# Kernel optimization log

Hardware: AMD Instinct MI355X
Metric: run time of the kernel (lower is better)

## Reference

```python
import jax, jax.numpy as jnp
import numpy as np

B, S, D, H = 2, 2048, 1024, 16


def setup_inputs() -> dict:
    key = jax.random.key(0)
    kq, kk, kv, kw = jax.random.split(key, 4)
    Q = jax.random.normal(kq, (B, S, D), dtype=jnp.float32)
    K = jax.random.normal(kk, (B, S, D), dtype=jnp.float32)
    V = jax.random.normal(kv, (B, S, D), dtype=jnp.float32)
    Wo = jax.random.normal(kw, (D, D), dtype=jnp.float32) * (1.0 / np.sqrt(D))
    return {"Q": Q, "K": K, "V": V, "Wo": Wo, "num_heads": H}


def reference(Q, K, V, Wo, num_heads):
    b, s, d = Q.shape
    dk = d // num_heads
    # split heads: [B,S,D] -> [B,H,S,dk]
    q = Q.reshape(b, s, num_heads, dk).transpose(0, 2, 1, 3)
    k = K.reshape(b, s, num_heads, dk).transpose(0, 2, 1, 3)
    v = V.reshape(b, s, num_heads, dk).transpose(0, 2, 1, 3)
    scale = 1.0 / jnp.sqrt(jnp.asarray(dk, dtype=q.dtype))
    logits = jnp.einsum('bhqd,bhkd->bhqk', q, k) * scale  # [B,H,S,S]
    probs = jax.nn.softmax(logits, axis=-1).astype(q.dtype)
    o = jnp.einsum('bhqk,bhkd->bhqd', probs, v)  # [B,H,S,dk]
    o = o.transpose(0, 2, 1, 3).reshape(b, s, d)  # concat heads
    # O = einsum('d dkh, ... dkh -> ... d', Wo, scores) == scores @ Wo^T
    return jnp.einsum('dk,bsk->bsd', Wo, o)
```

## Files before the change

kernel.cpp:

```cpp
#include <hip/hip_runtime.h>
#include <hip/hip_bf16.h>

#define B_ 2
#define S_ 2048
#define D_ 1024
#define H_ 16
#define DK_ 64

typedef __hip_bfloat16 bf16;
typedef short v8s __attribute__((ext_vector_type(8)));
typedef short v4s __attribute__((ext_vector_type(4)));
typedef float v4f __attribute__((ext_vector_type(4)));
typedef float v16f __attribute__((ext_vector_type(16)));
typedef int   v4i __attribute__((ext_vector_type(4)));
typedef int   v2i __attribute__((ext_vector_type(2)));

static __device__ __forceinline__ v16f mfma32(v8s a, v8s b, v16f c) {
  return __builtin_amdgcn_mfma_f32_32x32x16_bf16(a, b, c, 0, 0, 0);
}
static __device__ __forceinline__ void gl2lds16(const void* g, void* l) {
  __builtin_amdgcn_global_load_lds((const __attribute__((address_space(1))) void*)g,
                                   (__attribute__((address_space(3))) void*)l,
                                   16, 0, 0);
}
static __device__ __forceinline__ short f2bf(float x) {
  return (short)__builtin_bit_cast(unsigned short, __float2bfloat16(x));
}
static __device__ __forceinline__ int pk2f(float lo, float hi) {
  unsigned a = __builtin_bit_cast(unsigned, lo) + 0x8000u;
  unsigned b = __builtin_bit_cast(unsigned, hi) + 0x8000u;
  return (int)__builtin_amdgcn_perm(b, a, 0x07060302u);
}
static __device__ __forceinline__ float bf2f(short s) {
  return __builtin_bit_cast(float, ((unsigned)(unsigned short)s) << 16);
}

__global__ __launch_bounds__(256) void pre_kernel(
    const float* __restrict__ K, const float* __restrict__ V,
    const float* __restrict__ Wo, bf16* __restrict__ Kb,
    bf16* __restrict__ Vt, bf16* __restrict__ Wb)
{
  __shared__ __align__(16) bf16 td[64 * 72];
  const int t = threadIdx.x;
  const int bx = blockIdx.x;

  if (bx < 2048) {
    const int idx = bx * 256 + t;
    const int seg = idx & 7;
    const int rest = idx >> 3;
    const int h = rest & 15;
    const int bs = rest >> 4;
    const float* src = K + (size_t)bs * D_ + h * 64 + seg * 8;
    v4f x = *(const v4f*)src, y = *(const v4f*)(src + 4);
    v8s r;
    r[0]=f2bf(x[0]); r[1]=f2bf(x[1]); r[2]=f2bf(x[2]); r[3]=f2bf(x[3]);
    r[4]=f2bf(y[0]); r[5]=f2bf(y[1]); r[6]=f2bf(y[2]); r[7]=f2bf(y[3]);
    const int b = bs >> 11, s = bs & 2047;
    *(v8s*)(Kb + ((size_t)(b * H_ + h) * S_ + s) * DK_ + seg * 8) = r;
  } else if (bx < 3072) {
    const int idx = bx - 2048;
    const int bh = idx >> 5, b = bh >> 4, h = bh & 15;
    const int s0 = (idx & 31) * 64;
    const int srow = t >> 2;
    const int cs = t & 3;
    const float* vp = V + (size_t)(b * S_ + s0 + srow) * D_ + h * 64 + cs * 16;
#pragma unroll
    for (int j = 0; j < 4; j++) {
      v4f x = *(const v4f*)(vp + j * 4);
#pragma unroll
      for (int jj = 0; jj < 4; jj++)
        td[(cs * 16 + j * 4 + jj) * 72 + srow] = __float2bfloat16(x[jj]);
    }
    __syncthreads();
    const int d = t >> 2;
#pragma unroll
    for (int a2 = 0; a2 < 4; a2++) {
      const int pos = cs * 16 + a2 * 4;
      const int g = pos >> 5;
      const int a = (pos >> 2) & 7;
      const int kbase = g * 32 + ((a >> 2) << 4) + ((a & 1) << 3) + (((a >> 1) & 1) << 2);
      v4s val = *(const v4s*)(td + d * 72 + kbase);
      *(v4s*)(Vt + ((size_t)bh * DK_ + d) * S_ + s0 + pos) = val;
    }
  } else {
    const int i = ((bx - 3072) * 256 + t) * 4;
    v4f a = *(const v4f*)(Wo + i);
    v4s r;
    r[0]=f2bf(a[0]); r[1]=f2bf(a[1]); r[2]=f2bf(a[2]); r[3]=f2bf(a[3]);
    *(v4s*)((short*)Wb + i) = r;
  }
}

__global__ __launch_bounds__(256, 4) void attn4_kernel(
    const float* __restrict__ Q, const bf16* __restrict__ Kb,
    const bf16* __restrict__ Vt, bf16* __restrict__ Op0,
    bf16* __restrict__ Op1, float* __restrict__ Lp)
{
  __shared__ __align__(16) bf16 kk[2][64 * 64];
  __shared__ __align__(16) bf16 vv[2][64 * 64];

  const int t = threadIdx.x;
  const int w = t >> 6, l = t & 63, h2 = l >> 5, ln = l & 31;

  const int bid = blockIdx.x;
  const int xcd = bid & 7;
  const int idx = bid >> 3;
  const int bh  = xcd * 4 + (idx >> 5);
  const int rest = idx & 31;
  const int qt = rest & 15, z = rest >> 4;

  const int b = bh >> 4, h = bh & 15;
  const int qbase = qt * 128 + w * 32;
  const int kb0 = z << 10;

  const bf16* Kbh = Kb + (size_t)bh * (S_ * DK_);
  const bf16* Vbh = Vt + (size_t)bh * (DK_ * S_);

  const float sc = 0.18033688011112042f;
  v8s bq[4];
  {
    const float* qp = Q + ((size_t)b * S_ + qbase + ln) * D_ + h * DK_ + h2 * 8;
#pragma unroll
    for (int c = 0; c < 4; c++) {
      v4f x = *(const v4f*)(qp + c * 16);
      v4f y = *(const v4f*)(qp + c * 16 + 4);
      v4i r = { pk2f(x[0]*sc, x[1]*sc), pk2f(x[2]*sc, x[3]*sc),
                pk2f(y[0]*sc, y[1]*sc), pk2f(y[2]*sc, y[3]*sc) };
      bq[c] = __builtin_bit_cast(v8s, r);
    }
  }

  v16f Z;
#pragma unroll
  for (int r = 0; r < 16; r++) Z[r] = 0.f;

  v16f accA, accB;
#pragma unroll
  for (int r = 0; r < 16; r++) { accA[r] = 0.f; accB[r] = 0.f; }
  float lpart = 0.f;

#pragma unroll
  for (int j = 0; j < 2; j++) {
    const int flat = j * 256 + t, row = flat >> 3, sp = flat & 7;
    gl2lds16(Kbh + (size_t)(kb0 + row) * DK_ + ((sp ^ (row & 7)) * 8), &kk[0][flat * 8]);
    gl2lds16(Vbh + (size_t)row * S_ + kb0 + ((sp ^ (row & 7)) * 8), &vv[0][flat * 8]);
  }

  int it = 0;
  for (int kb = kb0; kb < kb0 + 1024; kb += 64, it ^= 1) {
    __syncthreads();
    if (kb + 64 < kb0 + 1024) {
#pragma unroll
      for (int j = 0; j < 2; j++) {
        const int flat = j * 256 + t, row = flat >> 3, sp = flat & 7;
        gl2lds16(Kbh + (size_t)(kb + 64 + row) * DK_ + ((sp ^ (row & 7)) * 8),
                 &kk[it ^ 1][flat * 8]);
        gl2lds16(Vbh + (size_t)row * S_ + (kb + 64) + ((sp ^ (row & 7)) * 8),
                 &vv[it ^ 1][flat * 8]);
      }
    }
    const bf16* kc_ = kk[it];
    const bf16* vc_ = vv[it];

    v16f s0, s1;
    __builtin_amdgcn_s_setprio(1);
#pragma unroll
    for (int c = 0; c < 4; c++) {
      const int sd = 2 * c + h2;
      v8s a0 = *(const v8s*)(kc_ + ln * 64 + ((sd ^ (ln & 7)) * 8));
      v8s a1 = *(const v8s*)(kc_ + (32 + ln) * 64 + ((sd ^ (ln & 7)) * 8));
      if (c == 0) {
        s0 = mfma32(a0, bq[0], Z);
        s1 = mfma32(a1, bq[0], Z);
      } else {
        s0 = mfma32(a0, bq[c], s0);
        s1 = mfma32(a1, bq[c], s1);
      }
    }
    __builtin_amdgcn_s_setprio(0);

    float p0[16], p1[16];
#pragma unroll
    for (int r = 0; r < 16; r++) { p0[r] = exp2f(s0[r]); p1[r] = exp2f(s1[r]); }
    float suA = 0.f, suB = 0.f;
#pragma unroll
    for (int r = 0; r < 16; r++) { suA += p0[r]; suB += p1[r]; }
    lpart += suA + suB;

    v4i i00 = { pk2f(p0[0],p0[1]),  pk2f(p0[2],p0[3]),  pk2f(p0[4],p0[5]),  pk2f(p0[6],p0[7]) };
    v4i i01 = { pk2f(p0[8],p0[9]),  pk2f(p0[10],p0[11]),pk2f(p0[12],p0[13]),pk2f(p0[14],p0[15]) };
    v4i i10 = { pk2f(p1[0],p1[1]),  pk2f(p1[2],p1[3]),  pk2f(p1[4],p1[5]),  pk2f(p1[6],p1[7]) };
    v4i i11 = { pk2f(p1[8],p1[9]),  pk2f(p1[10],p1[11]),pk2f(p1[12],p1[13]),pk2f(p1[14],p1[15]) };
    v8s pb00 = __builtin_bit_cast(v8s, i00);
    v8s pb01 = __builtin_bit_cast(v8s, i01);
    v8s pb10 = __builtin_bit_cast(v8s, i10);
    v8s pb11 = __builtin_bit_cast(v8s, i11);

    __builtin_amdgcn_s_setprio(1);
#pragma unroll
    for (int st = 0; st < 2; st++) {
#pragma unroll
      for (int kc = 0; kc < 2; kc++) {
        const int q = st * 4 + kc * 2 + h2;
        v8s avA = *(const v8s*)(vc_ + ln * 64 + ((q ^ (ln & 7)) * 8));
        v8s avB = *(const v8s*)(vc_ + (32 + ln) * 64 + ((q ^ (ln & 7)) * 8));
        v8s pb = st ? (kc ? pb11 : pb10) : (kc ? pb01 : pb00);
        accA = mfma32(avA, pb, accA);
        accB = mfma32(avB, pb, accB);
      }
    }
    __builtin_amdgcn_s_setprio(0);
  }

  __syncthreads();
  const float lfull = lpart + __shfl_xor(lpart, 32);
  bf16* epw = &kk[0][0] + w * 2048;
#pragma unroll
  for (int r = 0; r < 16; r += 4) {
    const int off = 4 * h2;
    const int sgA = (r >> 2) ^ (ln & 3);
    const int sgB = 4 + sgA;
    v2i pa = { pk2f(accA[r],   accA[r+1]),
               pk2f(accA[r+2], accA[r+3]) };
    v2i pb = { pk2f(accB[r],   accB[r+1]),
               pk2f(accB[r+2], accB[r+3]) };
    *(v2i*)(epw + ln * 64 + sgA * 8 + off) = pa;
    *(v2i*)(epw + ln * 64 + sgB * 8 + off) = pb;
  }
  if (h2 == 0)
    Lp[((size_t)z * 32 + bh) * S_ + qbase + ln] = lfull;

  bf16* Op = z ? Op1 : Op0;
#pragma unroll
  for (int i = 0; i < 4; i++) {
    const int flat = i * 64 + l;
    const int qr = flat >> 3, sd = flat & 7;
    const int phys = ((sd & 3) ^ (qr & 3)) | (sd & 4);
    v8s val = *(const v8s*)(epw - w * 2048 + (w * 32 + qr) * 64 + phys * 8);
    *(v8s*)(Op + ((size_t)b * S_ + qbase - w * 32 + w * 32 + qr) * D_ + h * DK_ + sd * 8) = val;
  }
}

__global__ __launch_bounds__(256, 4) void projm_kernel(
    const bf16* __restrict__ Op0, const bf16* __restrict__ Op1,
    const float* __restrict__ Lp, const bf16* __restrict__ Wo,
    float* __restrict__ Out)
{
  __shared__ __align__(16) bf16 aa[2][64 * 64];
  __shared__ __align__(16) bf16 bb[2][64 * 64];

  const int t = threadIdx.x;
  const int w = t >> 6, l = t & 63, h2 = l >> 5, ln = l & 31;
  const int m0 = blockIdx.x * 64, n0 = blockIdx.y * 64;
  const int wm = (w & 1) * 32, wn = (w >> 1) * 32;
  const int b = m0 >> 11;

  v16f acc;
#pragma unroll
  for (int r = 0; r < 16; r++) acc[r] = 0.f;

  auto stage_load = [&](int k0, int j, v8s& a, v8s& c, float& inv) {
    const int flat = j * 256 + t, row = flat >> 3, sp = flat & 7;
    const int m = m0 + row, s = m & 2047;
    const int h = k0 >> 6;
    const size_t off = (size_t)m * D_ + k0 + ((sp ^ (row & 7)) * 8);
    a = *(const v8s*)(Op0 + off);
    c = *(const v8s*)(Op1 + off);
    const float l0 = Lp[(size_t)(b * H_ + h) * S_ + s];
    const float l1 = Lp[(size_t)(32 + b * H_ + h) * S_ + s];
    inv = 1.0f / (l0 + l1);
  };
  auto stage_write = [&](int buf, int j, v8s a, v8s c, float inv) {
    const int flat = j * 256 + t;
    v4i A = __builtin_bit_cast(v4i, a), C = __builtin_bit_cast(v4i, c);
    v4i r;
#pragma unroll
    for (int jj = 0; jj < 4; jj++) {
      const unsigned aw = (unsigned)A[jj], cw = (unsigned)C[jj];
      const float alo = __builtin_bit_cast(float, aw << 16);
      const float ahi = __builtin_bit_cast(float, aw & 0xffff0000u);
      const float clo = __builtin_bit_cast(float, cw << 16);
      const float chi = __builtin_bit_cast(float, cw & 0xffff0000u);
      r[jj] = pk2f((alo + clo) * inv, (ahi + chi) * inv);
    }
    *(v4i*)(&aa[buf][flat * 8]) = r;
  };

  v8s a0v, c0v, a1v, c1v; float i0v, i1v;
  stage_load(0, 0, a0v, c0v, i0v);
  stage_load(0, 1, a1v, c1v, i1v);
#pragma unroll
  for (int j = 0; j < 2; j++) {
    const int flat = j * 256 + t, row = flat >> 3, sp = flat & 7;
    gl2lds16(Wo + (size_t)(n0 + row) * D_ + ((sp ^ (row & 7)) * 8), &bb[0][flat * 8]);
  }
  stage_write(0, 0, a0v, c0v, i0v);
  stage_write(0, 1, a1v, c1v, i1v);

  int it = 0;
  for (int k0 = 0; k0 < D_; k0 += 64, it ^= 1) {
    __syncthreads();
    const bool nxt = (k0 + 64 < D_);
    if (nxt) {
      stage_load(k0 + 64, 0, a0v, c0v, i0v);
      stage_load(k0 + 64, 1, a1v, c1v, i1v);
#pragma unroll
      for (int j = 0; j < 2; j++) {
        const int flat = j * 256 + t, row = flat >> 3, sp = flat & 7;
        gl2lds16(Wo + (size_t)(n0 + row) * D_ + (k0 + 64) + ((sp ^ (row & 7)) * 8),
                 &bb[it ^ 1][flat * 8]);
      }
    }
    const bf16* ac = aa[it];
    const bf16* bc = bb[it];
#pragma unroll
    for (int c = 0; c < 4; c++) {
      const int sd = 2 * c + h2;
      v8s av = *(const v8s*)(ac + (wm + ln) * 64 + ((sd ^ (ln & 7)) * 8));
      v8s bv = *(const v8s*)(bc + (wn + ln) * 64 + ((sd ^ (ln & 7)) * 8));
      acc = mfma32(av, bv, acc);
    }
    if (nxt) {
      stage_write(it ^ 1, 0, a0v, c0v, i0v);
      stage_write(it ^ 1, 1, a1v, c1v, i1v);
    }
  }

#pragma unroll
  for (int r = 0; r < 16; r++) {
    const int row = m0 + wm + (r & 3) + 4 * h2 + 8 * (r >> 2);
    Out[(size_t)row * D_ + n0 + wn + ln] = acc[r];
  }
}

extern "C" void kernel_launch(void* const* d_in, const int* in_sizes, int n_in,
                              void* d_out, int out_size, void* d_ws, size_t ws_size,
                              hipStream_t stream) {
  (void)in_sizes; (void)n_in; (void)out_size; (void)ws_size;
  const float* Q  = (const float*)d_in[0];
  const float* K  = (const float*)d_in[1];
  const float* V  = (const float*)d_in[2];
  const float* Wo = (const float*)d_in[3];
  float* out = (float*)d_out;

  bf16* base = (bf16*)d_ws;
  bf16* kb   = base;
  bf16* vt   = base + (size_t)4  * 1024 * 1024;
  bf16* wo_b = base + (size_t)8  * 1024 * 1024;
  bf16* op0  = base + (size_t)9  * 1024 * 1024;
  bf16* op1  = base + (size_t)13 * 1024 * 1024;
  float* lp  = (float*)(base + (size_t)17 * 1024 * 1024);

  pre_kernel  <<<dim3(4096),       256, 0, stream>>>(K, V, Wo, kb, vt, wo_b);
  attn4_kernel<<<dim3(1024),       256, 0, stream>>>(Q, kb, vt, op0, op1, lp);
  projm_kernel<<<dim3(64, 16),     256, 0, stream>>>(op0, op1, lp, wo_b, out);
}
```

Baseline: 178.8 us.

## Triple-buffer K/V LDS staging with explicit vmcnt waits in attention kernel

Replaces the double-buffered K/V tile pipeline with a three-stage ring buffer that prefetches two tiles ahead. Each iteration waits with a partial s_waitcnt vmcnt instead of a full drain, then issues a raw barrier. A second barrier at the end of each iteration guards reuse of the buffer. The goal is to hide more global-to-LDS latency. In exchange, LDS use rises from 32KB to 48KB per block, which can cut occupancy below the 4 blocks requested by launch bounds, and there is one more barrier per iteration. A __syncthreads is also added before the epilogue reads the LDS scratch.

```diff
diff --git a/kernel.cpp b/kernel.cpp
--- a/kernel.cpp
+++ b/kernel.cpp
@@ -96,8 +96,8 @@
     const bf16* __restrict__ Vt, bf16* __restrict__ Op0,
     bf16* __restrict__ Op1, float* __restrict__ Lp)
 {
-  __shared__ __align__(16) bf16 kk[2][64 * 64];
-  __shared__ __align__(16) bf16 vv[2][64 * 64];
+  __shared__ __align__(16) bf16 kk[3][64 * 64];
+  __shared__ __align__(16) bf16 vv[3][64 * 64];
 
   const int t = threadIdx.x;
   const int w = t >> 6, l = t & 63, h2 = l >> 5, ln = l & 31;
@@ -139,28 +139,33 @@
   for (int r = 0; r < 16; r++) { accA[r] = 0.f; accB[r] = 0.f; }
   float lpart = 0.f;
 
-#pragma unroll
-  for (int j = 0; j < 2; j++) {
-    const int flat = j * 256 + t, row = flat >> 3, sp = flat & 7;
-    gl2lds16(Kbh + (size_t)(kb0 + row) * DK_ + ((sp ^ (row & 7)) * 8), &kk[0][flat * 8]);
-    gl2lds16(Vbh + (size_t)row * S_ + kb0 + ((sp ^ (row & 7)) * 8), &vv[0][flat * 8]);
-  }
-
-  int it = 0;
-  for (int kb = kb0; kb < kb0 + 1024; kb += 64, it ^= 1) {
-    __syncthreads();
-    if (kb + 64 < kb0 + 1024) {
-#pragma unroll
-      for (int j = 0; j < 2; j++) {
-        const int flat = j * 256 + t, row = flat >> 3, sp = flat & 7;
-        gl2lds16(Kbh + (size_t)(kb + 64 + row) * DK_ + ((sp ^ (row & 7)) * 8),
-                 &kk[it ^ 1][flat * 8]);
-        gl2lds16(Vbh + (size_t)row * S_ + (kb + 64) + ((sp ^ (row & 7)) * 8),
-                 &vv[it ^ 1][flat * 8]);
-      }
-    }
-    const bf16* kc_ = kk[it];
-    const bf16* vc_ = vv[it];
+  auto stage = [&](int kbt, int buf) {
+#pragma unroll
+    for (int j = 0; j < 2; j++) {
+      const int flat = j * 256 + t, row = flat >> 3, sp = flat & 7;
+      gl2lds16(Kbh + (size_t)(kbt + row) * DK_ + ((sp ^ (row & 7)) * 8), &kk[buf][flat * 8]);
+      gl2lds16(Vbh + (size_t)row * S_ + kbt + ((sp ^ (row & 7)) * 8), &vv[buf][flat * 8]);
+    }
+  };
+
+  stage(kb0, 0);
+  stage(kb0 + 64, 1);
+
+  int ib = 0;
+  for (int kb = kb0; kb < kb0 + 1024; kb += 64) {
+    if (kb + 64 < kb0 + 1024)
+      asm volatile("s_waitcnt vmcnt(4)" ::: "memory");
+    else
+      asm volatile("s_waitcnt vmcnt(0)" ::: "memory");
+    __builtin_amdgcn_s_barrier();
+
+    if (kb + 128 < kb0 + 1024) {
+      int sb = ib + 2; if (sb >= 3) sb -= 3;
+      stage(kb + 128, sb);
+    }
+
+    const bf16* kc_ = kk[ib];
+    const bf16* vc_ = vv[ib];
 
     v16f s0, s1;
     __builtin_amdgcn_s_setprio(1);
@@ -210,6 +215,9 @@
       }
     }
     __builtin_amdgcn_s_setprio(0);
+
+    __builtin_amdgcn_s_barrier();
+    ib = (ib == 2) ? 0 : ib + 1;
   }
 
   __syncthreads();
@@ -230,6 +238,7 @@
   if (h2 == 0)
     Lp[((size_t)z * 32 + bh) * S_ + qbase + ln] = lfull;
 
+  __syncthreads();
   bf16* Op = z ? Op1 : Op0;
 #pragma unroll
   for (int i = 0; i < 4; i++) {
```

After: 190.5 us. 1.07x slower.
